# Optimization experiments

Measured on AMD Instinct MI355X. Metric: run time of the kernel, lower is better.

## Reference

```python
import jax, jax.numpy as jnp
import numpy as np

B, S, D, H, HID = 2, 2048, 512, 8, 2048
DH = D // H
EPS = 1e-5


def _ln(x, g, b):
    mu = jnp.mean(x, axis=-1, keepdims=True)
    var = jnp.mean(jnp.square(x - mu), axis=-1, keepdims=True)
    return (x - mu) * jax.lax.rsqrt(var + EPS) * g + b


def setup_inputs() -> dict:
    key = jax.random.key(0)
    ks = jax.random.split(key, 12)
    s = 0.02
    return {
        "x": jax.random.normal(ks[0], (B, S, D), jnp.float32),
        "prev": jax.random.normal(ks[1], (B, H, S, S), jnp.float32),
        # weights stored as [in, out]
        "kqv_w": jax.random.normal(ks[2], (D, 3 * D), jnp.float32) * s,
        "kqv_b": jnp.zeros((3 * D,), jnp.float32),
        "out_w": jax.random.normal(ks[3], (D, D), jnp.float32) * s,
        "out_b": jnp.zeros((D,), jnp.float32),
        "fc1_w": jax.random.normal(ks[4], (D, HID), jnp.float32) * s,
        "fc1_b": jnp.zeros((HID,), jnp.float32),
        "fc2_w": jax.random.normal(ks[5], (HID, D), jnp.float32) * s,
        "fc2_b": jnp.zeros((D,), jnp.float32),
        "ln1_g": jnp.ones((D,), jnp.float32),
        "ln1_b": jnp.zeros((D,), jnp.float32),
        "ln2_g": jnp.ones((D,), jnp.float32),
        "ln2_b": jnp.zeros((D,), jnp.float32),
    }


def reference(x, prev, kqv_w, kqv_b, out_w, out_b, fc1_w, fc1_b, fc2_w, fc2_b,
              ln1_g, ln1_b, ln2_g, ln2_b):
    scale = 1.0 / np.sqrt(DH)
    kqv = x @ kqv_w + kqv_b                      # [B,S,3D]
    # torch.chunk order: key, query, value
    k, q, v = jnp.split(kqv, 3, axis=-1)
    k = k.reshape(B, S, H, DH)
    q = q.reshape(B, S, H, DH)
    v = v.reshape(B, S, H, DH)
    energy = scale * jnp.einsum('bqhd,bkhd->bhqk', q, k) + prev  # [B,H,S,S]
    attn = jax.nn.softmax(energy, axis=-1)
    ctx = jnp.einsum('bhqk,bkhd->bqhd', attn, v).reshape(B, S, D)
    attn_out = ctx @ out_w + out_b
    h = _ln(attn_out + x, ln1_g, ln1_b)          # post-norm 1
    ff = jax.nn.gelu(h @ fc1_w + fc1_b, approximate=False) @ fc2_w + fc2_b
    out = _ln(ff + h, ln2_g, ln2_b)              # post-norm 2
    return (out, energy)
```

## Files before the change

kernel.cpp:

```cpp
#include <hip/hip_runtime.h>
#include <math.h>

#define S_ 2048
#define D_ 512
#define H_ 8
#define DH_ 64
#define HID_ 2048
#define NT_ 4096
#define K3D_ 1536

typedef unsigned short u16;
typedef __bf16 bf16x8 __attribute__((ext_vector_type(8)));
typedef float f32x4 __attribute__((ext_vector_type(4)));

typedef const __attribute__((address_space(1))) unsigned int* gas_p;
typedef __attribute__((address_space(3))) unsigned int* las_p;

__device__ __forceinline__ float b2f(u16 u) {
  union { unsigned int i; float f; } v; v.i = ((unsigned int)u) << 16; return v.f;
}
__device__ __forceinline__ u16 f2b(float f) {
  union { float f; unsigned int i; } v; v.f = f;
  unsigned int u = v.i;
  u += 0x7fffu + ((u >> 16) & 1u);
  return (u16)(u >> 16);
}

__global__ __launch_bounds__(256) void cvt_kernel(
    const float* __restrict__ in, u16* __restrict__ out, int n8) {
  int i = blockIdx.x * 256 + threadIdx.x;
  if (i >= n8) return;
  size_t base = (size_t)i * 8;
  float4 a = *(const float4*)(in + base);
  float4 b = *(const float4*)(in + base + 4);
  u16 ov[8] = {f2b(a.x), f2b(a.y), f2b(a.z), f2b(a.w),
               f2b(b.x), f2b(b.y), f2b(b.z), f2b(b.w)};
  *(uint4*)(out + base) = *(uint4*)ov;
}

__global__ __launch_bounds__(256) void transpose_kernel(
    const float* __restrict__ in, u16* __restrict__ out, int R, int C) {
  int idx = blockIdx.x * 256 + threadIdx.x;
  if (idx >= R * C) return;
  int r = idx / C, c = idx % C;
  out[(size_t)c * R + r] = f2b(in[idx]);
}

__global__ __launch_bounds__(256) void vt_kernel(
    const u16* __restrict__ kqv, u16* __restrict__ vt) {
  int bh = blockIdx.y, b = bh >> 3, h = bh & 7;
  const u16* V = kqv + (size_t)b * S_ * K3D_ + 2 * D_ + h * DH_;
  u16* O = vt + (size_t)bh * DH_ * S_;
  int idx = blockIdx.x * 256 + threadIdx.x;
  int r = idx >> 6, c = idx & 63;
  O[(size_t)c * S_ + r] = V[(size_t)r * K3D_ + c];
}

template<int BN>
__global__ __launch_bounds__(256) void gemm_glds(
    const u16* __restrict__ A, const u16* __restrict__ Bt,
    const float* __restrict__ bias, u16* __restrict__ C,
    int K, int lda, int ldb, int ldc, int gelu) {
  constexpr int BM = 128;
  constexpr int NF = BN / 32;
  constexpr int A_LOADS = BM / 64;
  constexpr int B_LOADS = BN / 64;

  __shared__ alignas(16) u16 As[BM * 32];
  __shared__ alignas(16) u16 Bs[BN * 32];

  int t = threadIdx.x;
  int w = t >> 6, lane = t & 63, quad = lane >> 4, l16 = lane & 15;
  int wr = w >> 1, wc = w & 1;
  int tile_m = blockIdx.y * BM, tile_n = blockIdx.x * BN;

  int srow = lane >> 2, schunk = (lane & 3) * 8;

  f32x4 acc[4][NF];
#pragma unroll
  for (int i = 0; i < 4; ++i)
#pragma unroll
    for (int n = 0; n < NF; ++n) acc[i][n] = (f32x4){0.f, 0.f, 0.f, 0.f};

  for (int kb = 0; kb < K; kb += 32) {
    __syncthreads();
#pragma unroll
    for (int j = 0; j < A_LOADS; ++j) {
      int jj = w * A_LOADS + j;
      const u16* g = A + (size_t)(tile_m + jj * 16 + srow) * lda + kb + schunk;
      __builtin_amdgcn_global_load_lds((gas_p)(const void*)g,
                                       (las_p)(void*)(As + jj * 512), 16, 0, 0);
    }
#pragma unroll
    for (int j = 0; j < B_LOADS; ++j) {
      int jj = w * B_LOADS + j;
      const u16* g = Bt + (size_t)(tile_n + jj * 16 + srow) * ldb + kb + schunk;
      __builtin_amdgcn_global_load_lds((gas_p)(const void*)g,
                                       (las_p)(void*)(Bs + jj * 512), 16, 0, 0);
    }
    __syncthreads();

    bf16x8 af[4], bfr[NF];
#pragma unroll
    for (int i = 0; i < 4; ++i)
      af[i] = *(const bf16x8*)(&As[(wr * 64 + i * 16 + l16) * 32 + quad * 8]);
#pragma unroll
    for (int n = 0; n < NF; ++n)
      bfr[n] = *(const bf16x8*)(&Bs[(wc * (BN / 2) + n * 16 + l16) * 32 + quad * 8]);
#pragma unroll
    for (int i = 0; i < 4; ++i)
#pragma unroll
      for (int n = 0; n < NF; ++n)
        acc[i][n] = __builtin_amdgcn_mfma_f32_16x16x32_bf16(af[i], bfr[n], acc[i][n], 0, 0, 0);
  }

#pragma unroll
  for (int n = 0; n < NF; ++n) {
    int col = tile_n + wc * (BN / 2) + n * 16 + l16;
    float bcol = bias[col];
#pragma unroll
    for (int i = 0; i < 4; ++i) {
#pragma unroll
      for (int r = 0; r < 4; ++r) {
        int row = tile_m + wr * 64 + i * 16 + quad * 4 + r;
        float v = acc[i][n][r] + bcol;
        if (gelu) v = 0.5f * v * (1.f + erff(v * 0.70710678118654752f));
        C[(size_t)row * ldc + col] = f2b(v);
      }
    }
  }
}

__global__ __launch_bounds__(256) void fused_attn(
    const u16* __restrict__ kqv, const u16* __restrict__ vt,
    const float* __restrict__ prev, float* __restrict__ energy,
    u16* __restrict__ ctx) {
  int bh = blockIdx.y, b = bh >> 3, h = bh & 7;
  int qbase = blockIdx.x * 64;

  const u16* Qp  = kqv + (size_t)b * S_ * K3D_ + D_ + h * DH_;
  const u16* Kp  = kqv + (size_t)b * S_ * K3D_ + h * DH_;
  const u16* Vtp = vt + (size_t)bh * DH_ * S_;
  const float* Pvp = prev + (size_t)bh * S_ * S_;
  float* Ep = energy + (size_t)bh * S_ * S_;

  int t = threadIdx.x;
  int w = t >> 6, lane = t & 63, quad = lane >> 4, l16 = lane & 15;

  __shared__ alignas(16) u16 KsB[2][64 * 72];
  __shared__ alignas(16) u16 VsB[2][64 * 72];
  __shared__ alignas(16) float Es[4][16 * 68];
  __shared__ alignas(16) u16 Pt[4][16 * 72];
  __shared__ float m_s[4][16];
  __shared__ float l_s[4][16];
  __shared__ float r_s[4][16];

  bf16x8 qf0, qf1;
  {
    const u16* qrow = Qp + (size_t)(qbase + w * 16 + l16) * K3D_;
    qf0 = *(const bf16x8*)(qrow + quad * 8);
    qf1 = *(const bf16x8*)(qrow + 32 + quad * 8);
  }

  if (lane < 16) { m_s[w][lane] = -1e30f; l_s[w][lane] = 0.f; }

  f32x4 oa[4];
#pragma unroll
  for (int i = 0; i < 4; ++i) oa[i] = (f32x4){0.f, 0.f, 0.f, 0.f};

  int c0 = t * 2, c1 = c0 + 1;
  int kr0 = c0 >> 3, ko0 = (c0 & 7) * 8;
  int kr1 = c1 >> 3, ko1 = (c1 & 7) * 8;

  {
    uint4 ka0 = *(const uint4*)(Kp + (size_t)kr0 * K3D_ + ko0);
    uint4 ka1 = *(const uint4*)(Kp + (size_t)kr1 * K3D_ + ko1);
    uint4 va0 = *(const uint4*)(Vtp + (size_t)kr0 * S_ + ko0);
    uint4 va1 = *(const uint4*)(Vtp + (size_t)kr1 * S_ + ko1);
    *(uint4*)(&KsB[0][kr0 * 72 + ko0]) = ka0;
    *(uint4*)(&KsB[0][kr1 * 72 + ko1]) = ka1;
    *(uint4*)(&VsB[0][kr0 * 72 + ko0]) = va0;
    *(uint4*)(&VsB[0][kr1 * 72 + ko1]) = va1;
  }
  __syncthreads();

  for (int it = 0; it < 32; ++it) {
    int cur = it & 1;
    int kb = it * 64;

    uint4 ka0, ka1, va0, va1;
    if (it < 31) {
      int kn = kb + 64;
      ka0 = *(const uint4*)(Kp + (size_t)(kn + kr0) * K3D_ + ko0);
      ka1 = *(const uint4*)(Kp + (size_t)(kn + kr1) * K3D_ + ko1);
      va0 = *(const uint4*)(Vtp + (size_t)kr0 * S_ + kn + ko0);
      va1 = *(const uint4*)(Vtp + (size_t)kr1 * S_ + kn + ko1);
    }

    const u16* Ks = KsB[cur];
    const u16* Vs = VsB[cur];

    f32x4 sa[4];
#pragma unroll
    for (int i = 0; i < 4; ++i) sa[i] = (f32x4){0.f, 0.f, 0.f, 0.f};
#pragma unroll
    for (int kc = 0; kc < 2; ++kc) {
      bf16x8 a = kc ? qf1 : qf0;
#pragma unroll
      for (int nt = 0; nt < 4; ++nt) {
        bf16x8 bk = *(const bf16x8*)(&Ks[(nt * 16 + l16) * 72 + kc * 32 + quad * 8]);
        sa[nt] = __builtin_amdgcn_mfma_f32_16x16x32_bf16(a, bk, sa[nt], 0, 0, 0);
      }
    }

#pragma unroll
    for (int nt = 0; nt < 4; ++nt)
#pragma unroll
      for (int r = 0; r < 4; ++r)
        Es[w][(quad * 4 + r) * 68 + nt * 16 + l16] = sa[nt][r] * 0.125f;
    asm volatile("" ::: "memory");

    float4 ek[4];
    float mt[4];
#pragma unroll
    for (int r4 = 0; r4 < 4; ++r4) {
      int row = r4 * 4 + quad;
      float4 e4 = *(const float4*)(&Es[w][row * 68 + l16 * 4]);
      size_t goff = (size_t)(qbase + w * 16 + row) * S_ + kb + l16 * 4;
      float4 p4 = *(const float4*)(Pvp + goff);
      e4.x += p4.x; e4.y += p4.y; e4.z += p4.z; e4.w += p4.w;
      *(float4*)(Ep + goff) = e4;
      ek[r4] = e4;
      mt[r4] = fmaxf(fmaxf(e4.x, e4.y), fmaxf(e4.z, e4.w));
    }
#pragma unroll
    for (int r4 = 0; r4 < 4; ++r4)
#pragma unroll
      for (int off = 1; off < 16; off <<= 1)
        mt[r4] = fmaxf(mt[r4], __shfl_xor(mt[r4], off, 16));
    if (l16 == 0) {
#pragma unroll
      for (int r4 = 0; r4 < 4; ++r4) {
        int row = r4 * 4 + quad;
        float mo = m_s[w][row];
        float mn = fmaxf(mo, mt[r4]);
        r_s[w][row] = __expf(mo - mn);
        m_s[w][row] = mn;
      }
    }
    asm volatile("" ::: "memory");

    float ls[4];
#pragma unroll
    for (int r4 = 0; r4 < 4; ++r4) {
      int row = r4 * 4 + quad;
      float mrow = m_s[w][row];
      float4 e4 = ek[r4];
      float p0 = __expf(e4.x - mrow), p1 = __expf(e4.y - mrow);
      float p2 = __expf(e4.z - mrow), p3 = __expf(e4.w - mrow);
      ls[r4] = (p0 + p1) + (p2 + p3);
      u16 pb[4] = {f2b(p0), f2b(p1), f2b(p2), f2b(p3)};
      *(uint2*)(&Pt[w][row * 72 + l16 * 4]) = *(uint2*)pb;
    }
#pragma unroll
    for (int r4 = 0; r4 < 4; ++r4)
#pragma unroll
      for (int off = 1; off < 16; off <<= 1)
        ls[r4] += __shfl_xor(ls[r4], off, 16);
    if (l16 == 0) {
#pragma unroll
      for (int r4 = 0; r4 < 4; ++r4) {
        int row = r4 * 4 + quad;
        l_s[w][row] = l_s[w][row] * r_s[w][row] + ls[r4];
      }
    }
#pragma unroll
    for (int rr = 0; rr < 4; ++rr) {
      float rf = r_s[w][quad * 4 + rr];
#pragma unroll
      for (int nt = 0; nt < 4; ++nt) oa[nt][rr] *= rf;
    }
    asm volatile("" ::: "memory");

#pragma unroll
    for (int kc = 0; kc < 2; ++kc) {
      bf16x8 a = *(const bf16x8*)(&Pt[w][l16 * 72 + kc * 32 + quad * 8]);
#pragma unroll
      for (int nt = 0; nt < 4; ++nt) {
        bf16x8 bv = *(const bf16x8*)(&Vs[(nt * 16 + l16) * 72 + kc * 32 + quad * 8]);
        oa[nt] = __builtin_amdgcn_mfma_f32_16x16x32_bf16(a, bv, oa[nt], 0, 0, 0);
      }
    }

    if (it < 31) {
      int nxt = cur ^ 1;
      *(uint4*)(&KsB[nxt][kr0 * 72 + ko0]) = ka0;
      *(uint4*)(&KsB[nxt][kr1 * 72 + ko1]) = ka1;
      *(uint4*)(&VsB[nxt][kr0 * 72 + ko0]) = va0;
      *(uint4*)(&VsB[nxt][kr1 * 72 + ko1]) = va1;
      __syncthreads();
    }
  }

  asm volatile("" ::: "memory");
  float il[4];
#pragma unroll
  for (int rr = 0; rr < 4; ++rr) il[rr] = 1.f / l_s[w][quad * 4 + rr];
#pragma unroll
  for (int nt = 0; nt < 4; ++nt) {
    int col = h * DH_ + nt * 16 + l16;
#pragma unroll
    for (int rr = 0; rr < 4; ++rr) {
      size_t row = (size_t)b * S_ + qbase + w * 16 + quad * 4 + rr;
      ctx[row * D_ + col] = f2b(oa[nt][rr] * il[rr]);
    }
  }
}

__global__ __launch_bounds__(256) void ln_kernel(
    const u16* __restrict__ a, const void* __restrict__ rsrc,
    const float* __restrict__ g, const float* __restrict__ be,
    void* __restrict__ o, int r_f32, int o_f32) {
  int row = blockIdx.x * 4 + (threadIdx.x >> 6);
  int lane = threadIdx.x & 63;
  size_t base = (size_t)row * D_ + lane * 8;
  uint4 av = *(const uint4*)(a + base);
  const u16* ap = (const u16*)&av;
  float rv[8];
  if (r_f32) {
    float4 r0 = *(const float4*)((const float*)rsrc + base);
    float4 r1 = *(const float4*)((const float*)rsrc + base + 4);
    rv[0] = r0.x; rv[1] = r0.y; rv[2] = r0.z; rv[3] = r0.w;
    rv[4] = r1.x; rv[5] = r1.y; rv[6] = r1.z; rv[7] = r1.w;
  } else {
    uint4 rr = *(const uint4*)((const u16*)rsrc + base);
    const u16* rp = (const u16*)&rr;
#pragma unroll
    for (int j = 0; j < 8; ++j) rv[j] = b2f(rp[j]);
  }
  float tv[8], s = 0.f, sq = 0.f;
#pragma unroll
  for (int j = 0; j < 8; ++j) {
    float xx = b2f(ap[j]) + rv[j];
    tv[j] = xx; s += xx; sq += xx * xx;
  }
#pragma unroll
  for (int off = 32; off; off >>= 1) {
    s  += __shfl_xor(s, off);
    sq += __shfl_xor(sq, off);
  }
  float mu  = s * (1.f / 512.f);
  float var = fmaxf(sq * (1.f / 512.f) - mu * mu, 0.f);
  float wv  = rsqrtf(var + 1e-5f);
  float4 g0 = *(const float4*)(g + lane * 8);
  float4 g1 = *(const float4*)(g + lane * 8 + 4);
  float4 b0 = *(const float4*)(be + lane * 8);
  float4 b1 = *(const float4*)(be + lane * 8 + 4);
  float gv[8] = {g0.x, g0.y, g0.z, g0.w, g1.x, g1.y, g1.z, g1.w};
  float bv[8] = {b0.x, b0.y, b0.z, b0.w, b1.x, b1.y, b1.z, b1.w};
  if (o_f32) {
    float ov[8];
#pragma unroll
    for (int j = 0; j < 8; ++j) ov[j] = (tv[j] - mu) * wv * gv[j] + bv[j];
    *(float4*)((float*)o + base)     = *(float4*)(ov);
    *(float4*)((float*)o + base + 4) = *(float4*)(ov + 4);
  } else {
    u16 ov[8];
#pragma unroll
    for (int j = 0; j < 8; ++j) ov[j] = f2b((tv[j] - mu) * wv * gv[j] + bv[j]);
    *(uint4*)((u16*)o + base) = *(uint4*)ov;
  }
}

extern "C" void kernel_launch(void* const* d_in, const int* in_sizes, int n_in,
                              void* d_out, int out_size, void* d_ws, size_t ws_size,
                              hipStream_t stream) {
  const float* x     = (const float*)d_in[0];
  const float* prev  = (const float*)d_in[1];
  const float* kqv_w = (const float*)d_in[2];
  const float* kqv_b = (const float*)d_in[3];
  const float* out_w = (const float*)d_in[4];
  const float* out_b = (const float*)d_in[5];
  const float* fc1_w = (const float*)d_in[6];
  const float* fc1_b = (const float*)d_in[7];
  const float* fc2_w = (const float*)d_in[8];
  const float* fc2_b = (const float*)d_in[9];
  const float* ln1_g = (const float*)d_in[10];
  const float* ln1_b = (const float*)d_in[11];
  const float* ln2_g = (const float*)d_in[12];
  const float* ln2_b = (const float*)d_in[13];

  float* outp   = (float*)d_out;
  float* energy = outp + (size_t)NT_ * D_;

  u16* ws = (u16*)d_ws;
  u16* R0 = ws;
  u16* R2 = R0 + (size_t)8388608;
  u16* R3 = R2 + (size_t)2097152;
  u16* R4 = R3 + (size_t)2097152;
  u16* WA = R4 + (size_t)2097152;

  u16* kqv    = R0;
  u16* vt     = R0 + (size_t)6291456;
  u16* attn   = R0;
  u16* ff     = R0;
  u16* ctx    = R2;  u16* f2     = R2;
  u16* hbuf   = R3;
  u16* xb     = R4;
  u16* fc1_wt = R4;  u16* fc2_wt = R4 + (size_t)1048576;
  u16* kqv_wt = WA;  u16* out_wt = WA;

  cvt_kernel<<<(NT_ * D_ / 8 + 255) / 256, 256, 0, stream>>>(x, xb, NT_ * D_ / 8);
  transpose_kernel<<<(D_ * K3D_ + 255) / 256, 256, 0, stream>>>(kqv_w, kqv_wt, D_, K3D_);

  gemm_glds<128><<<dim3(K3D_ / 128, NT_ / 128, 1), 256, 0, stream>>>(
      xb, kqv_wt, kqv_b, kqv, D_, D_, D_, K3D_, 0);

  transpose_kernel<<<(D_ * HID_ + 255) / 256, 256, 0, stream>>>(fc1_w, fc1_wt, D_, HID_);
  transpose_kernel<<<(HID_ * D_ + 255) / 256, 256, 0, stream>>>(fc2_w, fc2_wt, HID_, D_);
  transpose_kernel<<<(D_ * D_ + 255) / 256, 256, 0, stream>>>(out_w, out_wt, D_, D_);

  vt_kernel<<<dim3((S_ * DH_) / 256, 16), 256, 0, stream>>>(kqv, vt);

  fused_attn<<<dim3(S_ / 64, 16), 256, 0, stream>>>(kqv, vt, prev, energy, ctx);

  gemm_glds<64><<<dim3(D_ / 64, NT_ / 128, 1), 256, 0, stream>>>(
      ctx, out_wt, out_b, attn, D_, D_, D_, D_, 0);

  ln_kernel<<<NT_ / 4, 256, 0, stream>>>(attn, x, ln1_g, ln1_b, hbuf, 1, 0);

  gemm_glds<128><<<dim3(HID_ / 128, NT_ / 128, 1), 256, 0, stream>>>(
      hbuf, fc1_wt, fc1_b, ff, D_, D_, D_, HID_, 1);

  gemm_glds<64><<<dim3(D_ / 64, NT_ / 128, 1), 256, 0, stream>>>(
      ff, fc2_wt, fc2_b, f2, HID_, HID_, HID_, D_, 0);

  ln_kernel<<<NT_ / 4, 256, 0, stream>>>(f2, hbuf, ln2_g, ln2_b, outp, 0, 1);
}
```

Measured before the change: 678.7 us.

## Tile transposes via LDS, double-buffer GEMM tiles, prefetch prev in attention

Replaces the naive scalar weight transposes and the V-transpose with LDS-tiled versions that make both global reads and writes coalesced. The GEMM gains a double-buffered LDS stage, so the next K-slice is fetched while MFMAs run on the current one, removing one barrier per iteration. The attention kernel loads the prev bias tile for the next key block one iteration ahead to hide global latency. Costs are doubled GEMM LDS footprint and extra registers in attention, which may reduce occupancy.

```diff
diff --git a/kernel.cpp b/kernel.cpp
--- a/kernel.cpp
+++ b/kernel.cpp
@@ -38,22 +38,43 @@
   *(uint4*)(out + base) = *(uint4*)ov;
 }
 
-__global__ __launch_bounds__(256) void transpose_kernel(
+__global__ __launch_bounds__(256) void transpose_t32(
     const float* __restrict__ in, u16* __restrict__ out, int R, int C) {
-  int idx = blockIdx.x * 256 + threadIdx.x;
-  if (idx >= R * C) return;
-  int r = idx / C, c = idx % C;
-  out[(size_t)c * R + r] = f2b(in[idx]);
-}
-
-__global__ __launch_bounds__(256) void vt_kernel(
+  __shared__ u16 tile[32][40];
+  int r0 = blockIdx.y * 32, c0 = blockIdx.x * 32;
+  int t = threadIdx.x;
+  int r = t >> 3, c4 = (t & 7) * 4;
+  float4 v = *(const float4*)(in + (size_t)(r0 + r) * C + c0 + c4);
+  tile[r][c4 + 0] = f2b(v.x);
+  tile[r][c4 + 1] = f2b(v.y);
+  tile[r][c4 + 2] = f2b(v.z);
+  tile[r][c4 + 3] = f2b(v.w);
+  __syncthreads();
+  int c = t >> 3, r4 = (t & 7) * 4;
+  u16 o[4] = {tile[r4 + 0][c], tile[r4 + 1][c], tile[r4 + 2][c], tile[r4 + 3][c]};
+  *(uint2*)(out + (size_t)(c0 + c) * R + r0 + r4) = *(uint2*)o;
+}
+
+__global__ __launch_bounds__(256) void vt_tiled(
     const u16* __restrict__ kqv, u16* __restrict__ vt) {
   int bh = blockIdx.y, b = bh >> 3, h = bh & 7;
   const u16* V = kqv + (size_t)b * S_ * K3D_ + 2 * D_ + h * DH_;
   u16* O = vt + (size_t)bh * DH_ * S_;
-  int idx = blockIdx.x * 256 + threadIdx.x;
-  int r = idx >> 6, c = idx & 63;
-  O[(size_t)c * S_ + r] = V[(size_t)r * K3D_ + c];
+  __shared__ u16 tile[64][72];
+  int k0 = blockIdx.x * 64;
+  int t = threadIdx.x;
+  int kr = t >> 2, ko = (t & 3) * 16;
+  uint4 v0 = *(const uint4*)(V + (size_t)(k0 + kr) * K3D_ + ko);
+  uint4 v1 = *(const uint4*)(V + (size_t)(k0 + kr) * K3D_ + ko + 8);
+  *(uint4*)(&tile[kr][ko]) = v0;
+  *(uint4*)(&tile[kr][ko + 8]) = v1;
+  __syncthreads();
+  int dh = t >> 2, kk = (t & 3) * 16;
+  u16 o[16];
+#pragma unroll
+  for (int j = 0; j < 16; ++j) o[j] = tile[kk + j][dh];
+  *(uint4*)(O + (size_t)dh * S_ + k0 + kk)     = ((uint4*)o)[0];
+  *(uint4*)(O + (size_t)dh * S_ + k0 + kk + 8) = ((uint4*)o)[1];
 }
 
 template<int BN>
@@ -66,14 +87,13 @@
   constexpr int A_LOADS = BM / 64;
   constexpr int B_LOADS = BN / 64;
 
-  __shared__ alignas(16) u16 As[BM * 32];
-  __shared__ alignas(16) u16 Bs[BN * 32];
+  __shared__ alignas(16) u16 As[2][BM * 32];
+  __shared__ alignas(16) u16 Bs[2][BN * 32];
 
   int t = threadIdx.x;
   int w = t >> 6, lane = t & 63, quad = lane >> 4, l16 = lane & 15;
   int wr = w >> 1, wc = w & 1;
   int tile_m = blockIdx.y * BM, tile_n = blockIdx.x * BN;
-
   int srow = lane >> 2, schunk = (lane & 3) * 8;
 
   f32x4 acc[4][NF];
@@ -82,37 +102,48 @@
 #pragma unroll
     for (int n = 0; n < NF; ++n) acc[i][n] = (f32x4){0.f, 0.f, 0.f, 0.f};
 
-  for (int kb = 0; kb < K; kb += 32) {
-    __syncthreads();
-#pragma unroll
-    for (int j = 0; j < A_LOADS; ++j) {
-      int jj = w * A_LOADS + j;
-      const u16* g = A + (size_t)(tile_m + jj * 16 + srow) * lda + kb + schunk;
-      __builtin_amdgcn_global_load_lds((gas_p)(const void*)g,
-                                       (las_p)(void*)(As + jj * 512), 16, 0, 0);
-    }
-#pragma unroll
-    for (int j = 0; j < B_LOADS; ++j) {
-      int jj = w * B_LOADS + j;
-      const u16* g = Bt + (size_t)(tile_n + jj * 16 + srow) * ldb + kb + schunk;
-      __builtin_amdgcn_global_load_lds((gas_p)(const void*)g,
-                                       (las_p)(void*)(Bs + jj * 512), 16, 0, 0);
-    }
-    __syncthreads();
+#define STAGE_TILE(buf, kb)                                                   \
+  {                                                                           \
+    _Pragma("unroll")                                                         \
+    for (int j = 0; j < A_LOADS; ++j) {                                       \
+      int jj = w * A_LOADS + j;                                               \
+      const u16* g = A + (size_t)(tile_m + jj * 16 + srow) * lda + (kb) + schunk; \
+      __builtin_amdgcn_global_load_lds((gas_p)(const void*)g,                 \
+          (las_p)(void*)(&As[buf][jj * 512]), 16, 0, 0);                      \
+    }                                                                         \
+    _Pragma("unroll")                                                         \
+    for (int j = 0; j < B_LOADS; ++j) {                                       \
+      int jj = w * B_LOADS + j;                                               \
+      const u16* g = Bt + (size_t)(tile_n + jj * 16 + srow) * ldb + (kb) + schunk; \
+      __builtin_amdgcn_global_load_lds((gas_p)(const void*)g,                 \
+          (las_p)(void*)(&Bs[buf][jj * 512]), 16, 0, 0);                      \
+    }                                                                         \
+  }
+
+  STAGE_TILE(0, 0);
+  __syncthreads();
+
+  int nsteps = K >> 5;
+  for (int s = 0; s < nsteps; ++s) {
+    int cur = s & 1;
+    if (s + 1 < nsteps) STAGE_TILE(cur ^ 1, (s + 1) * 32);
 
     bf16x8 af[4], bfr[NF];
 #pragma unroll
     for (int i = 0; i < 4; ++i)
-      af[i] = *(const bf16x8*)(&As[(wr * 64 + i * 16 + l16) * 32 + quad * 8]);
+      af[i] = *(const bf16x8*)(&As[cur][(wr * 64 + i * 16 + l16) * 32 + quad * 8]);
 #pragma unroll
     for (int n = 0; n < NF; ++n)
-      bfr[n] = *(const bf16x8*)(&Bs[(wc * (BN / 2) + n * 16 + l16) * 32 + quad * 8]);
+      bfr[n] = *(const bf16x8*)(&Bs[cur][(wc * (BN / 2) + n * 16 + l16) * 32 + quad * 8]);
 #pragma unroll
     for (int i = 0; i < 4; ++i)
 #pragma unroll
       for (int n = 0; n < NF; ++n)
         acc[i][n] = __builtin_amdgcn_mfma_f32_16x16x32_bf16(af[i], bfr[n], acc[i][n], 0, 0, 0);
-  }
+
+    if (s + 1 < nsteps) __syncthreads();
+  }
+#undef STAGE_TILE
 
 #pragma unroll
   for (int n = 0; n < NF; ++n) {
@@ -171,6 +202,13 @@
   int c0 = t * 2, c1 = c0 + 1;
   int kr0 = c0 >> 3, ko0 = (c0 & 7) * 8;
   int kr1 = c1 >> 3, ko1 = (c1 & 7) * 8;
+
+  float4 pv[4];
+#pragma unroll
+  for (int r4 = 0; r4 < 4; ++r4) {
+    int row = r4 * 4 + quad;
+    pv[r4] = *(const float4*)(Pvp + (size_t)(qbase + w * 16 + row) * S_ + l16 * 4);
+  }
 
   {
     uint4 ka0 = *(const uint4*)(Kp + (size_t)kr0 * K3D_ + ko0);
@@ -227,11 +265,18 @@
       int row = r4 * 4 + quad;
       float4 e4 = *(const float4*)(&Es[w][row * 68 + l16 * 4]);
       size_t goff = (size_t)(qbase + w * 16 + row) * S_ + kb + l16 * 4;
-      float4 p4 = *(const float4*)(Pvp + goff);
+      float4 p4 = pv[r4];
       e4.x += p4.x; e4.y += p4.y; e4.z += p4.z; e4.w += p4.w;
       *(float4*)(Ep + goff) = e4;
       ek[r4] = e4;
       mt[r4] = fmaxf(fmaxf(e4.x, e4.y), fmaxf(e4.z, e4.w));
+    }
+    if (it < 31) {
+#pragma unroll
+      for (int r4 = 0; r4 < 4; ++r4) {
+        int row = r4 * 4 + quad;
+        pv[r4] = *(const float4*)(Pvp + (size_t)(qbase + w * 16 + row) * S_ + kb + 64 + l16 * 4);
+      }
     }
 #pragma unroll
     for (int r4 = 0; r4 < 4; ++r4)
@@ -411,16 +456,16 @@
   u16* kqv_wt = WA;  u16* out_wt = WA;
 
   cvt_kernel<<<(NT_ * D_ / 8 + 255) / 256, 256, 0, stream>>>(x, xb, NT_ * D_ / 8);
-  transpose_kernel<<<(D_ * K3D_ + 255) / 256, 256, 0, stream>>>(kqv_w, kqv_wt, D_, K3D_);
+  transpose_t32<<<dim3(K3D_ / 32, D_ / 32), 256, 0, stream>>>(kqv_w, kqv_wt, D_, K3D_);
 
   gemm_glds<128><<<dim3(K3D_ / 128, NT_ / 128, 1), 256, 0, stream>>>(
       xb, kqv_wt, kqv_b, kqv, D_, D_, D_, K3D_, 0);
 
-  transpose_kernel<<<(D_ * HID_ + 255) / 256, 256, 0, stream>>>(fc1_w, fc1_wt, D_, HID_);
-  transpose_kernel<<<(HID_ * D_ + 255) / 256, 256, 0, stream>>>(fc2_w, fc2_wt, HID_, D_);
-  transpose_kernel<<<(D_ * D_ + 255) / 256, 256, 0, stream>>>(out_w, out_wt, D_, D_);
-
-  vt_kernel<<<dim3((S_ * DH_) / 256, 16), 256, 0, stream>>>(kqv, vt);
+  transpose_t32<<<dim3(HID_ / 32, D_ / 32), 256, 0, stream>>>(fc1_w, fc1_wt, D_, HID_);
+  transpose_t32<<<dim3(D_ / 32, HID_ / 32), 256, 0, stream>>>(fc2_w, fc2_wt, HID_, D_);
+  transpose_t32<<<dim3(D_ / 32, D_ / 32), 256, 0, stream>>>(out_w, out_wt, D_, D_);
+
+  vt_tiled<<<dim3(S_ / 64, 16), 256, 0, stream>>>(kqv, vt);
 
   fused_attn<<<dim3(S_ / 64, 16), 256, 0, stream>>>(kqv, vt, prev, energy, ctx);
 
```

Result: faster. 633.6 us (-6.6%).
